# Kernel tuning notes

Measured on AMD Instinct MI355X. Metric: run time of the kernel, lower is better.

## Reference

```python
import jax, jax.numpy as jnp
import numpy as np

B, T, C = 2, 2048, 1024
NH = 16
HD = C // NH
SCALE = 1.0 / np.sqrt(HD).astype(np.float32)


def setup_inputs() -> dict:
    key = jax.random.key(0)
    k1, k2, k3 = jax.random.split(key, 3)
    x = jax.random.normal(k1, (B, T, C), dtype=jnp.float32)
    # torch Linear stores weight (out,in) and computes x @ W^T; we store the
    # transposed (in,out) layout directly, scaled like default init.
    w_qkv = jax.random.normal(k2, (C, 3 * C), dtype=jnp.float32) * (1.0 / np.sqrt(C))
    w_proj = jax.random.normal(k3, (C, C), dtype=jnp.float32) * (1.0 / np.sqrt(C))
    return {"x": x, "w_qkv": w_qkv, "w_proj": w_proj}


def reference(x, w_qkv, w_proj):
    b, t, c = x.shape
    qkv = x @ w_qkv                                  # (b, t, 3c)
    q, k, v = jnp.split(qkv, 3, axis=-1)
    q = q.reshape(b, t, NH, HD)
    k = k.reshape(b, t, NH, HD)
    v = v.reshape(b, t, NH, HD)
    # scores: (b, nh, t, t) — full materialization, faithful to the original
    att = jnp.einsum("bthd,bshd->bhts", q, k) * SCALE
    causal = jnp.tril(jnp.ones((t, t), dtype=bool))  # (t, t)
    neg = jnp.finfo(att.dtype).min
    att = jnp.where(causal[None, None, :, :], att, neg)
    weights = jax.nn.softmax(att, axis=-1)
    y = jnp.einsum("bhts,bshd->bthd", weights, v).reshape(b, t, c)
    y = y @ w_proj
    return y
```

## Files before the change

kernel.cpp:

```cpp
#include <hip/hip_runtime.h>
#include <hip/hip_bf16.h>
#include <stdint.h>

typedef __bf16 bf16x8 __attribute__((ext_vector_type(8)));
typedef float f32x4 __attribute__((ext_vector_type(4)));
typedef unsigned short us4v __attribute__((ext_vector_type(4)));
typedef unsigned short us8v __attribute__((ext_vector_type(8)));

#define B_   2
#define T_   2048
#define C_   1024
#define NH_  16
#define HD_  64

__device__ __forceinline__ unsigned short f2bf(float f) {
  unsigned int u = __builtin_bit_cast(unsigned int, f);
  u += 0x7fffu + ((u >> 16) & 1u);
  return (unsigned short)(u >> 16);
}
__device__ __forceinline__ float bf2f(unsigned short u) {
  unsigned int x = ((unsigned int)u) << 16;
  return __builtin_bit_cast(float, x);
}

__device__ __forceinline__ void gload16(const void* g, void* l) {
  __builtin_amdgcn_global_load_lds(
      (const __attribute__((address_space(1))) unsigned int*)g,
      (__attribute__((address_space(3))) unsigned int*)l, 16, 0, 0);
}

__device__ __forceinline__ f32x4 mfma16(bf16x8 a, bf16x8 b, f32x4 c) {
  return __builtin_amdgcn_mfma_f32_16x16x32_bf16(a, b, c, 0, 0, 0);
}

__global__ __launch_bounds__(256) void cast_x_kernel(const float4* __restrict__ in,
                                                     us4v* __restrict__ out) {
  int i = blockIdx.x * 256 + threadIdx.x;
  float4 f = in[i];
  us4v o; o[0] = f2bf(f.x); o[1] = f2bf(f.y); o[2] = f2bf(f.z); o[3] = f2bf(f.w);
  out[i] = o;
}

__global__ __launch_bounds__(256) void transpose_cast_kernel(const float* __restrict__ w,
                                                             unsigned short* __restrict__ wT,
                                                             int K, int N) {
  __shared__ float tile[32][33];
  int n0 = blockIdx.x * 32, k0 = blockIdx.y * 32;
  int tx = threadIdx.x, ty = threadIdx.y;
  #pragma unroll
  for (int i = 0; i < 4; ++i)
    tile[ty + 8*i][tx] = w[(size_t)(k0 + ty + 8*i) * N + n0 + tx];
  __syncthreads();
  #pragma unroll
  for (int i = 0; i < 4; ++i)
    wT[(size_t)(n0 + ty + 8*i) * K + k0 + tx] = f2bf(tile[tx][ty + 8*i]);
}

__device__ __forceinline__ void gemm_core(const unsigned short* __restrict__ A,
                                          const unsigned short* __restrict__ Bt,
                                          int K, int m0, int n0,
                                          unsigned short* lA, unsigned short* lB,
                                          f32x4 acc[4][4]) {
  const int t = threadIdx.x;
  const int lane = t & 63, w = t >> 6;
  const int wm = w >> 1, wn = w & 1;
  const int g = lane >> 4, r16 = lane & 15;
  #pragma unroll
  for (int i = 0; i < 4; ++i)
    #pragma unroll
    for (int j = 0; j < 4; ++j) acc[i][j] = (f32x4){0.f, 0.f, 0.f, 0.f};

  for (int k0 = 0; k0 < K; k0 += 64) {
    #pragma unroll
    for (int i = 0; i < 4; ++i) {
      int slot = i * 256 + t;
      int r = slot >> 3, p = slot & 7;
      int q = p ^ (r & 7);
      gload16(A  + (size_t)(m0 + r) * K + k0 + q * 8, lA + slot * 8);
      gload16(Bt + (size_t)(n0 + r) * K + k0 + q * 8, lB + slot * 8);
    }
    asm volatile("s_waitcnt vmcnt(0)" ::: "memory");
    __syncthreads();

    bf16x8 af[4][2], bfr[4][2];
    #pragma unroll
    for (int mi = 0; mi < 4; ++mi)
      #pragma unroll
      for (int kk = 0; kk < 2; ++kk) {
        int r = wm * 64 + mi * 16 + r16;
        int ps = (kk * 4 + g) ^ (r & 7);
        af[mi][kk] = *(const bf16x8*)(lA + r * 64 + ps * 8);
      }
    #pragma unroll
    for (int ni = 0; ni < 4; ++ni)
      #pragma unroll
      for (int kk = 0; kk < 2; ++kk) {
        int r = wn * 64 + ni * 16 + r16;
        int ps = (kk * 4 + g) ^ (r & 7);
        bfr[ni][kk] = *(const bf16x8*)(lB + r * 64 + ps * 8);
      }
    #pragma unroll
    for (int mi = 0; mi < 4; ++mi)
      #pragma unroll
      for (int ni = 0; ni < 4; ++ni)
        #pragma unroll
        for (int kk = 0; kk < 2; ++kk)
          acc[mi][ni] = mfma16(af[mi][kk], bfr[ni][kk], acc[mi][ni]);
    __syncthreads();
  }
}

__device__ __forceinline__ int xcd_swz(int flat, int nwg) {
  int cpx = nwg >> 3;
  return (flat & 7) * cpx + (flat >> 3);
}

__global__ __launch_bounds__(256) void gemm_qkv_kernel(const unsigned short* __restrict__ xb,
                                                       const unsigned short* __restrict__ wT,
                                                       unsigned short* __restrict__ qb,
                                                       unsigned short* __restrict__ kb,
                                                       unsigned short* __restrict__ vb) {
  __shared__ unsigned short lA[128 * 64];
  __shared__ unsigned short lB[128 * 64];
  f32x4 acc[4][4];
  const int nbx = 3 * C_ / 128;
  int flat = xcd_swz(blockIdx.y * nbx + blockIdx.x, nbx * ((B_ * T_) / 128));
  const int m0 = (flat / nbx) * 128, n0 = (flat % nbx) * 128;
  gemm_core(xb, wT, C_, m0, n0, lA, lB, acc);
  const int t = threadIdx.x, lane = t & 63, w = t >> 6;
  const int wm = w >> 1, wn = w & 1, g = lane >> 4, r16 = lane & 15;
  #pragma unroll
  for (int mi = 0; mi < 4; ++mi)
    #pragma unroll
    for (int ni = 0; ni < 4; ++ni)
      #pragma unroll
      for (int j = 0; j < 4; ++j) {
        int gm = m0 + wm * 64 + mi * 16 + g * 4 + j;
        int gn = n0 + wn * 64 + ni * 16 + r16;
        int b = gm >> 11, tt = gm & 2047;
        int s = gn >> 10, rem = gn & 1023;
        int h = rem >> 6, d = rem & 63;
        unsigned short val = f2bf(acc[mi][ni][j]);
        size_t idx = ((size_t)(b * NH_ + h) * T_ + tt) * HD_ + d;
        if (s == 0)      qb[idx] = val;
        else if (s == 1) kb[idx] = val;
        else             vb[idx] = val;
      }
}

__global__ __launch_bounds__(256) void gemm_proj_kernel(const unsigned short* __restrict__ ab,
                                                        const unsigned short* __restrict__ wT,
                                                        float* __restrict__ out) {
  __shared__ unsigned short lA[128 * 64];
  __shared__ unsigned short lB[128 * 64];
  f32x4 acc[4][4];
  const int nbx = C_ / 128;
  int flat = xcd_swz(blockIdx.y * nbx + blockIdx.x, nbx * ((B_ * T_) / 128));
  const int m0 = (flat / nbx) * 128, n0 = (flat % nbx) * 128;
  gemm_core(ab, wT, C_, m0, n0, lA, lB, acc);
  const int t = threadIdx.x, lane = t & 63, w = t >> 6;
  const int wm = w >> 1, wn = w & 1, g = lane >> 4, r16 = lane & 15;
  #pragma unroll
  for (int mi = 0; mi < 4; ++mi)
    #pragma unroll
    for (int ni = 0; ni < 4; ++ni)
      #pragma unroll
      for (int j = 0; j < 4; ++j) {
        int gm = m0 + wm * 64 + mi * 16 + g * 4 + j;
        int gn = n0 + wn * 64 + ni * 16 + r16;
        out[(size_t)gm * C_ + gn] = acc[mi][ni][j];
      }
}

__global__ __launch_bounds__(256, 4) void attn_kernel(const unsigned short* __restrict__ qb,
                                                      const unsigned short* __restrict__ kb,
                                                      const unsigned short* __restrict__ vb,
                                                      unsigned short* __restrict__ ao,
                                                      unsigned short* __restrict__ partB,
                                                      float* __restrict__ mlbuf) {
  __shared__ unsigned short LDS[20480];
  const int L = blockIdx.x;
  const int inner = L >> 3;
  const int bh = (L & 7) * 4 + (inner / 48);
  const int bx = inner % 48;
  int tile, kvLo, kvHi, mode;
  if (bx < 16)      { tile = 16 + bx; kvLo = 0;  kvHi = 16;       mode = 1; }
  else if (bx < 32) { tile = 47 - bx; kvLo = 16; kvHi = tile + 1; mode = 2; }
  else              { tile = 47 - bx; kvLo = 0;  kvHi = tile + 1; mode = 0; }
  const int qt0 = tile * 64;
  const int len = kvHi - kvLo;
  const int t = threadIdx.x, lane = t & 63, w4 = t >> 6;
  const int g = lane >> 4, r16 = lane & 15;

  const unsigned short* Q  = qb + (size_t)bh * (T_ * HD_);
  const unsigned short* Kp = kb + (size_t)bh * (T_ * HD_);
  const unsigned short* Vp = vb + (size_t)bh * (T_ * HD_);

  bf16x8 qf[2];
  {
    int qrow = qt0 + w4 * 16 + r16;
    #pragma unroll
    for (int kk = 0; kk < 2; ++kk) {
      us8v raw = *(const us8v*)(Q + (size_t)qrow * HD_ + kk * 32 + g * 8);
      bf16x8 qv;
      #pragma unroll
      for (int j = 0; j < 8; ++j) qv[j] = (__bf16)(bf2f(raw[j]) * 0.125f);
      qf[kk] = qv;
    }
  }

  f32x4 o[4];
  #pragma unroll
  for (int c = 0; c < 4; ++c) o[c] = (f32x4){0.f, 0.f, 0.f, 0.f};
  float mrun = -__builtin_inff(), lrun = 0.f;

  const int kr0 = t >> 3,         kp0 = (t & 7) ^ (kr0 & 7);
  const int kr1 = (t + 256) >> 3, kp1 = (t & 7) ^ (kr1 & 7);
  const int colp = (lane & 32) | ((lane & 12) << 1) | ((lane >> 2) & 4) | (lane & 3);
  const int cslot = colp >> 3, cwithin = colp & 7;

  gload16(Kp + (size_t)(kvLo * 64 + kr0) * HD_ + kp0 * 8, LDS + t * 8);
  gload16(Kp + (size_t)(kvLo * 64 + kr1) * HD_ + kp1 * 8, LDS + (t + 256) * 8);
  us8v nvA0 = *(const us8v*)(Vp + (size_t)(kvLo * 64 + lane) * HD_ + w4 * 16);
  us8v nvA1 = *(const us8v*)(Vp + (size_t)(kvLo * 64 + lane) * HD_ + w4 * 16 + 8);
  us8v nvB0, nvB1;
  if (len > 1) {
    const int k1 = (kvLo + 1) * 64;
    gload16(Kp + (size_t)(k1 + kr0) * HD_ + kp0 * 8, LDS + 4096 + t * 8);
    gload16(Kp + (size_t)(k1 + kr1) * HD_ + kp1 * 8, LDS + 4096 + (t + 256) * 8);
    nvB0 = *(const us8v*)(Vp + (size_t)(k1 + lane) * HD_ + w4 * 16);
    nvB1 = *(const us8v*)(Vp + (size_t)(k1 + lane) * HD_ + w4 * 16 + 8);
  }

  for (int ii = 0; ii < len; ++ii) {
    const int it = kvLo + ii;
    const unsigned short* Kl = LDS + (ii % 3) * 4096;
    unsigned short* Vt = LDS + 12288 + (ii & 1) * 4096;

    if (ii + 1 < len) { asm volatile("s_waitcnt vmcnt(4)" ::: "memory"); }
    else              { asm volatile("s_waitcnt vmcnt(0)" ::: "memory"); }
    {
      us8v v0, v1;
      if (ii & 1) { v0 = nvB0; v1 = nvB1; } else { v0 = nvA0; v1 = nvA1; }
      #pragma unroll
      for (int u = 0; u < 8; ++u) {
        int d = w4 * 16 + u;
        Vt[d * 64 + ((cslot ^ u) << 3) + cwithin] = v0[u];
      }
      #pragma unroll
      for (int u = 0; u < 8; ++u) {
        int d = w4 * 16 + 8 + u;
        Vt[d * 64 + ((cslot ^ u) << 3) + cwithin] = v1[u];
      }
    }
    __syncthreads();

    if (ii + 2 < len) {
      const int kn = (it + 2) * 64;
      unsigned short* Kn = LDS + ((ii + 2) % 3) * 4096;
      gload16(Kp + (size_t)(kn + kr0) * HD_ + kp0 * 8, Kn + t * 8);
      gload16(Kp + (size_t)(kn + kr1) * HD_ + kp1 * 8, Kn + (t + 256) * 8);
      if (ii & 1) {
        nvB0 = *(const us8v*)(Vp + (size_t)(kn + lane) * HD_ + w4 * 16);
        nvB1 = *(const us8v*)(Vp + (size_t)(kn + lane) * HD_ + w4 * 16 + 8);
      } else {
        nvA0 = *(const us8v*)(Vp + (size_t)(kn + lane) * HD_ + w4 * 16);
        nvA1 = *(const us8v*)(Vp + (size_t)(kn + lane) * HD_ + w4 * 16 + 8);
      }
    }

    {
      f32x4 s4t[4];
      #pragma unroll
      for (int c = 0; c < 4; ++c) s4t[c] = (f32x4){0.f, 0.f, 0.f, 0.f};
      __builtin_amdgcn_s_setprio(1);
      #pragma unroll
      for (int c = 0; c < 4; ++c)
        #pragma unroll
        for (int kk = 0; kk < 2; ++kk) {
          int r = c * 16 + r16;
          int ps = (kk * 4 + g) ^ (r & 7);
          bf16x8 kf = *(const bf16x8*)(Kl + r * 64 + ps * 8);
          s4t[c] = mfma16(kf, qf[kk], s4t[c]);
        }
      __builtin_amdgcn_s_setprio(0);
      if (it == tile) {
        int qloc = w4 * 16 + r16;
        #pragma unroll
        for (int c = 0; c < 4; ++c)
          #pragma unroll
          for (int j = 0; j < 4; ++j)
            if (c * 16 + g * 4 + j > qloc) s4t[c][j] = -1e30f;
      }
      float mx = -1e30f;
      #pragma unroll
      for (int c = 0; c < 4; ++c)
        #pragma unroll
        for (int j = 0; j < 4; ++j) mx = fmaxf(mx, s4t[c][j]);
      mx = fmaxf(mx, __shfl_xor(mx, 16));
      mx = fmaxf(mx, __shfl_xor(mx, 32));
      float mn = fmaxf(mrun, mx);
      float alpha = __expf(mrun - mn);
      mrun = mn;
      float rs = 0.f;
      #pragma unroll
      for (int c = 0; c < 4; ++c)
        #pragma unroll
        for (int j = 0; j < 4; ++j) {
          float p = __expf(s4t[c][j] - mn);
          s4t[c][j] = p;
          rs += p;
        }
      rs += __shfl_xor(rs, 16);
      rs += __shfl_xor(rs, 32);
      lrun = lrun * alpha + rs;
      #pragma unroll
      for (int c = 0; c < 4; ++c)
        #pragma unroll
        for (int j = 0; j < 4; ++j) o[c][j] *= alpha;

      bf16x8 pf[2];
      #pragma unroll
      for (int kk = 0; kk < 2; ++kk) {
        bf16x8 p;
        #pragma unroll
        for (int j = 0; j < 4; ++j) {
          p[j]     = (__bf16)s4t[2 * kk][j];
          p[4 + j] = (__bf16)s4t[2 * kk + 1][j];
        }
        pf[kk] = p;
      }
      __builtin_amdgcn_s_setprio(1);
      #pragma unroll
      for (int c = 0; c < 4; ++c) {
        int rv = c * 16 + r16;
        #pragma unroll
        for (int kk = 0; kk < 2; ++kk) {
          int slot = (4 * kk + g) ^ (r16 & 7);
          bf16x8 vf = *(const bf16x8*)(Vt + rv * 64 + slot * 8);
          o[c] = mfma16(vf, pf[kk], o[c]);
        }
      }
      __builtin_amdgcn_s_setprio(0);
    }
  }

  if (mode && g == 0) {
    int prow = (bh * 16 + (tile - 16)) * 64 + w4 * 16 + r16;
    float* mlp = mlbuf + (size_t)prow * 4;
    if (mode == 1) { mlp[0] = mrun; mlp[1] = lrun; }
    else           { mlp[2] = mrun; mlp[3] = lrun; }
  }

  unsigned short* ep = LDS + (len % 3) * 4096 + w4 * 1024;
  float inv = 1.f / lrun;
  #pragma unroll
  for (int c = 0; c < 4; ++c) {
    us4v pk;
    #pragma unroll
    for (int j = 0; j < 4; ++j) pk[j] = f2bf(o[c][j] * inv);
    int slot = (4 * c + g) ^ r16;
    *(us4v*)(ep + r16 * 64 + slot * 4) = pk;
  }
  asm volatile("s_waitcnt lgkmcnt(0)" ::: "memory");
  __builtin_amdgcn_sched_barrier(0);
  {
    int q = lane >> 2, seg = lane & 3;
    us4v a0 = *(const us4v*)(ep + q * 64 + (((seg * 4 + 0) ^ q) & 15) * 4);
    us4v a1 = *(const us4v*)(ep + q * 64 + (((seg * 4 + 1) ^ q) & 15) * 4);
    us4v a2 = *(const us4v*)(ep + q * 64 + (((seg * 4 + 2) ^ q) & 15) * 4);
    us4v a3 = *(const us4v*)(ep + q * 64 + (((seg * 4 + 3) ^ q) & 15) * 4);
    us8v o0 = {a0[0],a0[1],a0[2],a0[3],a1[0],a1[1],a1[2],a1[3]};
    us8v o1 = {a2[0],a2[1],a2[2],a2[3],a3[0],a3[1],a3[2],a3[3]};
    if (mode != 2) {
      size_t rowg = (size_t)(bh >> 4) * T_ + qt0 + w4 * 16 + q;
      int colg = (bh & 15) * 64 + seg * 16;
      *(us8v*)(ao + rowg * C_ + colg)     = o0;
      *(us8v*)(ao + rowg * C_ + colg + 8) = o1;
    } else {
      size_t prow = (size_t)(bh * 16 + (tile - 16)) * 64 + w4 * 16 + q;
      *(us8v*)(partB + prow * 64 + seg * 16)     = o0;
      *(us8v*)(partB + prow * 64 + seg * 16 + 8) = o1;
    }
  }
}

__global__ __launch_bounds__(256) void attn_merge_kernel(unsigned short* __restrict__ ao,
                                                         const unsigned short* __restrict__ partB,
                                                         const float* __restrict__ mlbuf) {
  const int blk = blockIdx.x;
  const int bh = blk >> 4, ti = blk & 15;
  const int t = threadIdx.x;
  const int row = t >> 2, seg = t & 3;
  const size_t prow = (size_t)(bh * 16 + ti) * 64 + row;
  const float* mlp = mlbuf + prow * 4;
  float mA = mlp[0], lA = mlp[1], mB = mlp[2], lB = mlp[3];
  float m = fmaxf(mA, mB);
  float wA = lA * __expf(mA - m), wB = lB * __expf(mB - m);
  float rinv = 1.f / (wA + wB);
  wA *= rinv; wB *= rinv;
  size_t rowg = (size_t)(bh >> 4) * T_ + (16 + ti) * 64 + row;
  unsigned short* aop = ao + rowg * C_ + (bh & 15) * 64 + seg * 16;
  const unsigned short* obp = partB + prow * 64 + seg * 16;
  us8v oa0 = *(const us8v*)(aop);
  us8v oa1 = *(const us8v*)(aop + 8);
  us8v ob0 = *(const us8v*)(obp);
  us8v ob1 = *(const us8v*)(obp + 8);
  us8v r0, r1;
  #pragma unroll
  for (int j = 0; j < 8; ++j) {
    r0[j] = f2bf(bf2f(oa0[j]) * wA + bf2f(ob0[j]) * wB);
    r1[j] = f2bf(bf2f(oa1[j]) * wA + bf2f(ob1[j]) * wB);
  }
  *(us8v*)(aop)     = r0;
  *(us8v*)(aop + 8) = r1;
}

extern "C" void kernel_launch(void* const* d_in, const int* in_sizes, int n_in,
                              void* d_out, int out_size, void* d_ws, size_t ws_size,
                              hipStream_t stream) {
  const float* x      = (const float*)d_in[0];
  const float* w_qkv  = (const float*)d_in[1];
  const float* w_proj = (const float*)d_in[2];
  float* out = (float*)d_out;
  char* ws = (char*)d_ws;

  unsigned short* xb     = (unsigned short*)(ws);
  unsigned short* wqkvT  = (unsigned short*)(ws + 8388608);
  unsigned short* wprojT = (unsigned short*)(ws + 14680064);
  unsigned short* qb     = (unsigned short*)(ws + 16777216);
  unsigned short* kb     = (unsigned short*)(ws + 25165824);
  unsigned short* vb     = (unsigned short*)(ws + 33554432);
  unsigned short* ao     = xb;
  unsigned short* partB  = wqkvT;
  float*          mlbuf  = (float*)(ws + 8388608 + 4194304);

  cast_x_kernel<<<4096, 256, 0, stream>>>((const float4*)x, (us4v*)xb);
  transpose_cast_kernel<<<dim3(3 * C_ / 32, C_ / 32), dim3(32, 8), 0, stream>>>(
      w_qkv, wqkvT, C_, 3 * C_);
  transpose_cast_kernel<<<dim3(C_ / 32, C_ / 32), dim3(32, 8), 0, stream>>>(
      w_proj, wprojT, C_, C_);
  gemm_qkv_kernel<<<dim3(3 * C_ / 128, (B_ * T_) / 128), 256, 0, stream>>>(
      xb, wqkvT, qb, kb, vb);
  attn_kernel<<<dim3(1536), 256, 0, stream>>>(qb, kb, vb, ao, partB, mlbuf);
  attn_merge_kernel<<<512, 256, 0, stream>>>(ao, partB, mlbuf);
  gemm_proj_kernel<<<dim3(C_ / 128, (B_ * T_) / 128), 256, 0, stream>>>(
      ao, wprojT, out);
}
```

Baseline: 124.9 us.

## Process two query tiles per attention block, each wave handling 32 rows

Each attention block now covers two adjacent 64-row query tiles, with each wave computing 32 query rows (two 16-row MFMA groups) that share each loaded K/V fragment. The grid is halved and K/V tiles staged in LDS are reused across twice as many queries, cutting global and LDS traffic per unit of work. Waves assigned to the lower tile stop early through a per-wave iteration limit. The cost is more registers per thread (doubled accumulators and softmax state) and wave imbalance on the diagonal, which may lower occupancy under the launch bound of 4.

```diff
diff --git a/kernel.cpp b/kernel.cpp
--- a/kernel.cpp
+++ b/kernel.cpp
@@ -181,38 +181,46 @@
   __shared__ unsigned short LDS[20480];
   const int L = blockIdx.x;
   const int inner = L >> 3;
-  const int bh = (L & 7) * 4 + (inner / 48);
-  const int bx = inner % 48;
-  int tile, kvLo, kvHi, mode;
-  if (bx < 16)      { tile = 16 + bx; kvLo = 0;  kvHi = 16;       mode = 1; }
-  else if (bx < 32) { tile = 47 - bx; kvLo = 16; kvHi = tile + 1; mode = 2; }
-  else              { tile = 47 - bx; kvLo = 0;  kvHi = tile + 1; mode = 0; }
-  const int qt0 = tile * 64;
+  const int bh = (L & 7) * 4 + (inner / 24);
+  const int pidx = inner % 24;
+  const int pseg = pidx >> 3, pp = pidx & 7;
+  int t0, kvLo, kvHi, mode;
+  if (pseg == 0)      { t0 = 16 + 2 * pp;          kvLo = 0;  kvHi = 16;          mode = 1; }
+  else if (pseg == 1) { int q = 7 - pp; t0 = 2 * q;      kvLo = 0;  kvHi = 2 * q + 2;  mode = 0; }
+  else                { int q = 7 - pp; t0 = 16 + 2 * q; kvLo = 16; kvHi = 18 + 2 * q; mode = 2; }
   const int len = kvHi - kvLo;
   const int t = threadIdx.x, lane = t & 63, w4 = t >> 6;
   const int g = lane >> 4, r16 = lane & 15;
+  const int tsel = w4 >> 1, hsel = w4 & 1;
+  const int myTile = t0 + tsel;
+  const int qt0w = myTile * 64 + hsel * 32;
+  const int myLim = min(len, myTile + 1 - kvLo);
 
   const unsigned short* Q  = qb + (size_t)bh * (T_ * HD_);
   const unsigned short* Kp = kb + (size_t)bh * (T_ * HD_);
   const unsigned short* Vp = vb + (size_t)bh * (T_ * HD_);
 
-  bf16x8 qf[2];
-  {
-    int qrow = qt0 + w4 * 16 + r16;
+  bf16x8 qf[2][2];
+  #pragma unroll
+  for (int h = 0; h < 2; ++h) {
+    int qrow = qt0w + h * 16 + r16;
     #pragma unroll
     for (int kk = 0; kk < 2; ++kk) {
       us8v raw = *(const us8v*)(Q + (size_t)qrow * HD_ + kk * 32 + g * 8);
       bf16x8 qv;
       #pragma unroll
       for (int j = 0; j < 8; ++j) qv[j] = (__bf16)(bf2f(raw[j]) * 0.125f);
-      qf[kk] = qv;
-    }
-  }
-
-  f32x4 o[4];
-  #pragma unroll
-  for (int c = 0; c < 4; ++c) o[c] = (f32x4){0.f, 0.f, 0.f, 0.f};
-  float mrun = -__builtin_inff(), lrun = 0.f;
+      qf[h][kk] = qv;
+    }
+  }
+
+  f32x4 o[2][4];
+  #pragma unroll
+  for (int h = 0; h < 2; ++h)
+    #pragma unroll
+    for (int c = 0; c < 4; ++c) o[h][c] = (f32x4){0.f, 0.f, 0.f, 0.f};
+  float mrun[2] = {-__builtin_inff(), -__builtin_inff()};
+  float lrun[2] = {0.f, 0.f};
 
   const int kr0 = t >> 3,         kp0 = (t & 7) ^ (kr0 & 7);
   const int kr1 = (t + 256) >> 3, kp1 = (t & 7) ^ (kr1 & 7);
@@ -269,10 +277,12 @@
       }
     }
 
-    {
-      f32x4 s4t[4];
-      #pragma unroll
-      for (int c = 0; c < 4; ++c) s4t[c] = (f32x4){0.f, 0.f, 0.f, 0.f};
+    if (ii < myLim) {
+      f32x4 s4t[2][4];
+      #pragma unroll
+      for (int h = 0; h < 2; ++h)
+        #pragma unroll
+        for (int c = 0; c < 4; ++c) s4t[h][c] = (f32x4){0.f, 0.f, 0.f, 0.f};
       __builtin_amdgcn_s_setprio(1);
       #pragma unroll
       for (int c = 0; c < 4; ++c)
@@ -281,54 +291,60 @@
           int r = c * 16 + r16;
           int ps = (kk * 4 + g) ^ (r & 7);
           bf16x8 kf = *(const bf16x8*)(Kl + r * 64 + ps * 8);
-          s4t[c] = mfma16(kf, qf[kk], s4t[c]);
+          s4t[0][c] = mfma16(kf, qf[0][kk], s4t[0][c]);
+          s4t[1][c] = mfma16(kf, qf[1][kk], s4t[1][c]);
         }
       __builtin_amdgcn_s_setprio(0);
-      if (it == tile) {
-        int qloc = w4 * 16 + r16;
+      if (it == myTile) {
+        #pragma unroll
+        for (int h = 0; h < 2; ++h) {
+          int qloc = hsel * 32 + h * 16 + r16;
+          #pragma unroll
+          for (int c = 0; c < 4; ++c)
+            #pragma unroll
+            for (int j = 0; j < 4; ++j)
+              if (c * 16 + g * 4 + j > qloc) s4t[h][c][j] = -1e30f;
+        }
+      }
+      bf16x8 pf[2][2];
+      #pragma unroll
+      for (int h = 0; h < 2; ++h) {
+        float mx = -1e30f;
         #pragma unroll
         for (int c = 0; c < 4; ++c)
           #pragma unroll
-          for (int j = 0; j < 4; ++j)
-            if (c * 16 + g * 4 + j > qloc) s4t[c][j] = -1e30f;
-      }
-      float mx = -1e30f;
-      #pragma unroll
-      for (int c = 0; c < 4; ++c)
-        #pragma unroll
-        for (int j = 0; j < 4; ++j) mx = fmaxf(mx, s4t[c][j]);
-      mx = fmaxf(mx, __shfl_xor(mx, 16));
-      mx = fmaxf(mx, __shfl_xor(mx, 32));
-      float mn = fmaxf(mrun, mx);
-      float alpha = __expf(mrun - mn);
-      mrun = mn;
-      float rs = 0.f;
-      #pragma unroll
-      for (int c = 0; c < 4; ++c)
-        #pragma unroll
-        for (int j = 0; j < 4; ++j) {
-          float p = __expf(s4t[c][j] - mn);
-          s4t[c][j] = p;
-          rs += p;
+          for (int j = 0; j < 4; ++j) mx = fmaxf(mx, s4t[h][c][j]);
+        mx = fmaxf(mx, __shfl_xor(mx, 16));
+        mx = fmaxf(mx, __shfl_xor(mx, 32));
+        float mn = fmaxf(mrun[h], mx);
+        float alpha = __expf(mrun[h] - mn);
+        mrun[h] = mn;
+        float rs = 0.f;
+        #pragma unroll
+        for (int c = 0; c < 4; ++c)
+          #pragma unroll
+          for (int j = 0; j < 4; ++j) {
+            float p = __expf(s4t[h][c][j] - mn);
+            s4t[h][c][j] = p;
+            rs += p;
+          }
+        rs += __shfl_xor(rs, 16);
+        rs += __shfl_xor(rs, 32);
+        lrun[h] = lrun[h] * alpha + rs;
+        #pragma unroll
+        for (int c = 0; c < 4; ++c)
+          #pragma unroll
+          for (int j = 0; j < 4; ++j) o[h][c][j] *= alpha;
+        #pragma unroll
+        for (int kk = 0; kk < 2; ++kk) {
+          bf16x8 p;
+          #pragma unroll
+          for (int j = 0; j < 4; ++j) {
+            p[j]     = (__bf16)s4t[h][2 * kk][j];
+            p[4 + j] = (__bf16)s4t[h][2 * kk + 1][j];
+          }
+          pf[h][kk] = p;
         }
-      rs += __shfl_xor(rs, 16);
-      rs += __shfl_xor(rs, 32);
-      lrun = lrun * alpha + rs;
-      #pragma unroll
-      for (int c = 0; c < 4; ++c)
-        #pragma unroll
-        for (int j = 0; j < 4; ++j) o[c][j] *= alpha;
-
-      bf16x8 pf[2];
-      #pragma unroll
-      for (int kk = 0; kk < 2; ++kk) {
-        bf16x8 p;
-        #pragma unroll
-        for (int j = 0; j < 4; ++j) {
-          p[j]     = (__bf16)s4t[2 * kk][j];
-          p[4 + j] = (__bf16)s4t[2 * kk + 1][j];
-        }
-        pf[kk] = p;
       }
       __builtin_amdgcn_s_setprio(1);
       #pragma unroll
@@ -338,50 +354,55 @@
         for (int kk = 0; kk < 2; ++kk) {
           int slot = (4 * kk + g) ^ (r16 & 7);
           bf16x8 vf = *(const bf16x8*)(Vt + rv * 64 + slot * 8);
-          o[c] = mfma16(vf, pf[kk], o[c]);
+          o[0][c] = mfma16(vf, pf[0][kk], o[0][c]);
+          o[1][c] = mfma16(vf, pf[1][kk], o[1][c]);
         }
       }
       __builtin_amdgcn_s_setprio(0);
     }
   }
 
-  if (mode && g == 0) {
-    int prow = (bh * 16 + (tile - 16)) * 64 + w4 * 16 + r16;
-    float* mlp = mlbuf + (size_t)prow * 4;
-    if (mode == 1) { mlp[0] = mrun; mlp[1] = lrun; }
-    else           { mlp[2] = mrun; mlp[3] = lrun; }
-  }
-
   unsigned short* ep = LDS + (len % 3) * 4096 + w4 * 1024;
-  float inv = 1.f / lrun;
-  #pragma unroll
-  for (int c = 0; c < 4; ++c) {
-    us4v pk;
-    #pragma unroll
-    for (int j = 0; j < 4; ++j) pk[j] = f2bf(o[c][j] * inv);
-    int slot = (4 * c + g) ^ r16;
-    *(us4v*)(ep + r16 * 64 + slot * 4) = pk;
-  }
-  asm volatile("s_waitcnt lgkmcnt(0)" ::: "memory");
-  __builtin_amdgcn_sched_barrier(0);
-  {
-    int q = lane >> 2, seg = lane & 3;
-    us4v a0 = *(const us4v*)(ep + q * 64 + (((seg * 4 + 0) ^ q) & 15) * 4);
-    us4v a1 = *(const us4v*)(ep + q * 64 + (((seg * 4 + 1) ^ q) & 15) * 4);
-    us4v a2 = *(const us4v*)(ep + q * 64 + (((seg * 4 + 2) ^ q) & 15) * 4);
-    us4v a3 = *(const us4v*)(ep + q * 64 + (((seg * 4 + 3) ^ q) & 15) * 4);
-    us8v o0 = {a0[0],a0[1],a0[2],a0[3],a1[0],a1[1],a1[2],a1[3]};
-    us8v o1 = {a2[0],a2[1],a2[2],a2[3],a3[0],a3[1],a3[2],a3[3]};
-    if (mode != 2) {
-      size_t rowg = (size_t)(bh >> 4) * T_ + qt0 + w4 * 16 + q;
-      int colg = (bh & 15) * 64 + seg * 16;
-      *(us8v*)(ao + rowg * C_ + colg)     = o0;
-      *(us8v*)(ao + rowg * C_ + colg + 8) = o1;
-    } else {
-      size_t prow = (size_t)(bh * 16 + (tile - 16)) * 64 + w4 * 16 + q;
-      *(us8v*)(partB + prow * 64 + seg * 16)     = o0;
-      *(us8v*)(partB + prow * 64 + seg * 16 + 8) = o1;
-    }
+  #pragma unroll
+  for (int h = 0; h < 2; ++h) {
+    if (mode && g == 0) {
+      int prow = (bh * 16 + (myTile - 16)) * 64 + hsel * 32 + h * 16 + r16;
+      float* mlp = mlbuf + (size_t)prow * 4;
+      if (mode == 1) { mlp[0] = mrun[h]; mlp[1] = lrun[h]; }
+      else           { mlp[2] = mrun[h]; mlp[3] = lrun[h]; }
+    }
+    float inv = 1.f / lrun[h];
+    #pragma unroll
+    for (int c = 0; c < 4; ++c) {
+      us4v pk;
+      #pragma unroll
+      for (int j = 0; j < 4; ++j) pk[j] = f2bf(o[h][c][j] * inv);
+      int slot = (4 * c + g) ^ r16;
+      *(us4v*)(ep + r16 * 64 + slot * 4) = pk;
+    }
+    asm volatile("s_waitcnt lgkmcnt(0)" ::: "memory");
+    __builtin_amdgcn_sched_barrier(0);
+    {
+      int q = lane >> 2, seg = lane & 3;
+      us4v a0 = *(const us4v*)(ep + q * 64 + (((seg * 4 + 0) ^ q) & 15) * 4);
+      us4v a1 = *(const us4v*)(ep + q * 64 + (((seg * 4 + 1) ^ q) & 15) * 4);
+      us4v a2 = *(const us4v*)(ep + q * 64 + (((seg * 4 + 2) ^ q) & 15) * 4);
+      us4v a3 = *(const us4v*)(ep + q * 64 + (((seg * 4 + 3) ^ q) & 15) * 4);
+      us8v o0 = {a0[0],a0[1],a0[2],a0[3],a1[0],a1[1],a1[2],a1[3]};
+      us8v o1 = {a2[0],a2[1],a2[2],a2[3],a3[0],a3[1],a3[2],a3[3]};
+      if (mode != 2) {
+        size_t rowg = (size_t)(bh >> 4) * T_ + qt0w + h * 16 + q;
+        int colg = (bh & 15) * 64 + seg * 16;
+        *(us8v*)(ao + rowg * C_ + colg)     = o0;
+        *(us8v*)(ao + rowg * C_ + colg + 8) = o1;
+      } else {
+        size_t prow = (size_t)(bh * 16 + (myTile - 16)) * 64 + hsel * 32 + h * 16 + q;
+        *(us8v*)(partB + prow * 64 + seg * 16)     = o0;
+        *(us8v*)(partB + prow * 64 + seg * 16 + 8) = o1;
+      }
+    }
+    asm volatile("s_waitcnt lgkmcnt(0)" ::: "memory");
+    __builtin_amdgcn_sched_barrier(0);
   }
 }
 
@@ -442,7 +463,7 @@
       w_proj, wprojT, C_, C_);
   gemm_qkv_kernel<<<dim3(3 * C_ / 128, (B_ * T_) / 128), 256, 0, stream>>>(
       xb, wqkvT, qb, kb, vb);
-  attn_kernel<<<dim3(1536), 256, 0, stream>>>(qb, kb, vb, ao, partB, mlbuf);
+  attn_kernel<<<dim3(768), 256, 0, stream>>>(qb, kb, vb, ao, partB, mlbuf);
   attn_merge_kernel<<<512, 256, 0, stream>>>(ao, partB, mlbuf);
   gemm_proj_kernel<<<dim3(C_ / 128, (B_ * T_) / 128), 256, 0, stream>>>(
       ao, wprojT, out);
```

After: 141.4 us. +13.2%, slower.
